# Optimization experiments

Hardware: AMD Instinct MI355X
Metric: run time of the kernel (lower is better)

The kernel has to match this reference:

```python
import jax, jax.numpy as jnp
import numpy as np

B, S, H, D_MODEL, D_HEAD = 2, 2048, 12, 768, 64
INIT_RANGE = 0.02
IGNORE = -100000.0


def setup_inputs() -> dict:
    key = jax.random.key(0)
    ks = jax.random.split(key, 11)
    return {
        "normalized_resid_pre_q": jax.random.normal(ks[0], (B, S, H, D_MODEL), jnp.float32),
        "normalized_resid_pre_k": jax.random.normal(ks[1], (B, S, H, D_MODEL), jnp.float32),
        "normalized_resid_pre_v": jax.random.normal(ks[2], (B, S, H, D_MODEL), jnp.float32),
        "W_Q": jax.random.normal(ks[3], (H, D_MODEL, D_HEAD), jnp.float32) * INIT_RANGE,
        "b_Q": jnp.zeros((H, D_HEAD), jnp.float32),
        "W_K": jax.random.normal(ks[4], (H, D_MODEL, D_HEAD), jnp.float32) * INIT_RANGE,
        "b_K": jnp.zeros((H, D_HEAD), jnp.float32),
        "W_V": jax.random.normal(ks[5], (H, D_MODEL, D_HEAD), jnp.float32) * INIT_RANGE,
        "b_V": jnp.zeros((H, D_HEAD), jnp.float32),
        "W_O": jax.random.normal(ks[6], (H, D_HEAD, D_MODEL), jnp.float32) * INIT_RANGE,
        "b_O": jnp.zeros((D_MODEL,), jnp.float32),
    }


def reference(normalized_resid_pre_q, normalized_resid_pre_k, normalized_resid_pre_v,
              W_Q, b_Q, W_K, b_K, W_V, b_V, W_O, b_O):
    n_heads = W_Q.shape[0]
    d_head = W_Q.shape[-1]
    # per-head projections: input already carries a head axis
    q = jnp.einsum("bqhm,hmd->bqhd", normalized_resid_pre_q, W_Q) + b_Q
    k = jnp.einsum("bkhm,hmd->bkhd", normalized_resid_pre_k, W_K) + b_K
    v = jnp.einsum("bkhm,hmd->bkhd", normalized_resid_pre_v, W_V) + b_V
    scores = jnp.einsum("bqhd,bkhd->bhqk", q, k) / jnp.sqrt(jnp.float32(d_head))
    S_q, S_k = scores.shape[-2], scores.shape[-1]
    causal = jnp.triu(jnp.ones((S_q, S_k), bool), k=1)
    scores = jnp.where(causal, jnp.float32(IGNORE), scores)
    pattern = jax.nn.softmax(scores, axis=-1)
    z = jnp.einsum("bhqk,bkhd->bqhd", pattern, v)
    # output keeps the per-head axis; bias split evenly across heads
    attn_out = jnp.einsum("bqhd,hdm->bqhm", z, W_O) + b_O / n_heads
    return attn_out
```

## Files before the change

kernel.cpp:

```cpp
#include <hip/hip_runtime.h>
#include <stdint.h>

#define H 12
#define S 2048
#define BATCH 2
#define DM 768
#define DH 64

typedef __attribute__((ext_vector_type(4))) float f32x4;
typedef __attribute__((ext_vector_type(4))) short s16x4;
typedef __attribute__((ext_vector_type(8))) short s16x8;

static __device__ __forceinline__ short f2bf(float f) {
  uint32_t u = __builtin_bit_cast(uint32_t, f);
  uint32_t r = (u + 0x7FFFu + ((u >> 16) & 1u)) >> 16;
  return (short)r;
}

static __device__ __forceinline__ f32x4 zero4() {
  f32x4 v; v[0] = 0.f; v[1] = 0.f; v[2] = 0.f; v[3] = 0.f; return v;
}

#define GLD_LDS16(g, l)                                                              \
  __builtin_amdgcn_global_load_lds((__attribute__((address_space(1))) const void*)(g), \
                                   (__attribute__((address_space(3))) void*)(l), 16, 0, 0)

__global__ __launch_bounds__(256) void k_prep(const float* __restrict__ wq,
                                              const float* __restrict__ wk,
                                              const float* __restrict__ wv,
                                              const float* __restrict__ wo,
                                              short* __restrict__ wt,
                                              short* __restrict__ wot) {
  int tid = blockIdx.x * 256 + threadIdx.x;
  int nthr = gridDim.x * 256;
  const int NQKV = 3 * H * DM * DH;
  for (int i = tid; i < NQKV; i += nthr) {
    int n = i & 63;
    int k = (i >> 6) % DM;
    int rest = (i >> 6) / DM;
    int h = rest % H;
    int t = rest / H;
    const float* src = (t == 0 ? wq : t == 1 ? wk : wv);
    float v = src[((size_t)h * DM + k) * DH + n];
    wt[(((size_t)t * H + h) * DH + n) * DM + k] = f2bf(v);
  }
  const int NO = H * DH * DM;
  for (int i = tid; i < NO; i += nthr) {
    int m = i % DM;
    int d = (i / DM) % DH;
    int h = i / (DM * DH);
    wot[((size_t)h * DM + m) * DH + d] = f2bf(wo[((size_t)h * DH + d) * DM + m]);
  }
}

__global__ __launch_bounds__(256) void k_proj(
    const float* __restrict__ xq, const float* __restrict__ xk, const float* __restrict__ xv,
    const float* __restrict__ bq, const float* __restrict__ bk, const float* __restrict__ bv,
    const short* __restrict__ wt,
    short* __restrict__ q_ws, short* __restrict__ k_ws, short* __restrict__ vt_ws) {
  const int t = blockIdx.z;
  const int h = blockIdx.y;
  const int b = blockIdx.x >> 5;
  const int q0 = (blockIdx.x & 31) * 64;

  const float* x = (t == 0 ? xq : t == 1 ? xk : xv);
  const float* xbase = x + ((size_t)(b * S + q0) * H + h) * DM;
  const short* wbase = wt + ((size_t)t * H + h) * (size_t)DH * DM;

  __shared__ short A_sm[64 * 72];
  __shared__ short W_sm[64 * 64];

  const int tid = threadIdx.x;
  const int w = tid >> 6;
  const int l = tid & 63;
  const int g = l >> 4;
  const int m16 = l & 15;
  const int swz_src = ((l & 7) ^ (l >> 3)) * 8;

  f32x4 acc[4];
  for (int nt = 0; nt < 4; ++nt) acc[nt] = zero4();

  for (int kc = 0; kc < 12; ++kc) {
    if (kc) __syncthreads();
    for (int i = 0; i < 2; ++i) {
      int ch = w * 2 + i;
      int n = ch * 8 + (l >> 3);
      GLD_LDS16(wbase + (size_t)n * DM + kc * 64 + swz_src, (char*)W_sm + ch * 1024);
    }
    for (int p = 0; p < 4; ++p) {
      int q = p * 16 + (tid >> 4);
      int k0 = 4 * (tid & 15);
      f32x4 v = *(const f32x4*)(xbase + (size_t)q * (H * DM) + kc * 64 + k0);
      s16x4 o;
      o.x = f2bf(v[0]); o.y = f2bf(v[1]); o.z = f2bf(v[2]); o.w = f2bf(v[3]);
      *(s16x4*)(&A_sm[q * 72 + k0]) = o;
    }
    __syncthreads();
    for (int c = 0; c < 2; ++c) {
      int krow = 8 * g + 32 * c;
      s16x8 a = *(const s16x8*)(&A_sm[(16 * w + m16) * 72 + krow]);
      for (int nt = 0; nt < 4; ++nt) {
        int n = m16 + 16 * nt;
        int byte = (n * 128 + krow * 2) ^ ((n & 7) << 4);
        s16x8 bfr = *(const s16x8*)((const char*)W_sm + byte);
        acc[nt] = __builtin_amdgcn_mfma_f32_16x16x32_bf16(a, bfr, acc[nt], 0, 0, 0);
      }
    }
  }

  const float* bias = (t == 0 ? bq : t == 1 ? bk : bv) + h * DH;
  if (t < 2) {
    short* dst = (t == 0 ? q_ws : k_ws) + (size_t)(b * H + h) * S * DH;
    for (int nt = 0; nt < 4; ++nt) {
      int n = 16 * nt + m16;
      float bb = bias[n];
      for (int r = 0; r < 4; ++r) {
        int q = q0 + 16 * w + 4 * g + r;
        dst[(size_t)q * DH + n] = f2bf(acc[nt][r] + bb);
      }
    }
  } else {
    short* dst = vt_ws + (size_t)(b * H + h) * DH * S;
    for (int nt = 0; nt < 4; ++nt) {
      int n = 16 * nt + m16;
      float bb = bias[n];
      for (int r = 0; r < 4; ++r) {
        int q = q0 + 16 * w + 4 * g + r;
        dst[(size_t)n * S + q] = f2bf(acc[nt][r] + bb);
      }
    }
  }
}

__global__ __launch_bounds__(256) void k_attn(const short* __restrict__ q_ws,
                                              const short* __restrict__ k_ws,
                                              const short* __restrict__ vt_ws,
                                              short* __restrict__ z_ws) {
  const int b = blockIdx.z;
  const int h = blockIdx.y;
  const int q0 = blockIdx.x * 64;

  const size_t sl = (size_t)(b * H + h) * S * DH;
  const short* qs = q_ws + sl;
  const short* ks = k_ws + sl;
  const short* vs = vt_ws + sl;
  short* zs = z_ws + sl;

  __shared__ short K_sm[64 * 64];
  __shared__ short V_sm[64 * 64];
  __shared__ short P_sm[4][16 * 72];

  const int tid = threadIdx.x;
  const int w = tid >> 6;
  const int l = tid & 63;
  const int g = l >> 4;
  const int m16 = l & 15;
  const int swz_src = ((l & 7) ^ (l >> 3)) * 8;

  s16x8 qf[2];
  {
    int q = q0 + 16 * w + m16;
    qf[0] = *(const s16x8*)(qs + (size_t)q * DH + 8 * g);
    qf[1] = *(const s16x8*)(qs + (size_t)q * DH + 8 * g + 32);
  }

  f32x4 o_acc[4];
  float m_run[4], l_run[4], alpha[4];
  for (int nt = 0; nt < 4; ++nt) o_acc[nt] = zero4();
  for (int r = 0; r < 4; ++r) { m_run[r] = -3.0e38f; l_run[r] = 0.f; }

  const int ktiles = (q0 >> 6) + 1;
  for (int kt = 0; kt < ktiles; ++kt) {
    const int kv0 = kt * 64;
    if (kt) __syncthreads();
    for (int i = 0; i < 2; ++i) {
      int ch = w * 2 + i;
      int row = ch * 8 + (l >> 3);
      GLD_LDS16(ks + (size_t)(kv0 + row) * DH + swz_src, (char*)K_sm + ch * 1024);
      GLD_LDS16(vs + (size_t)row * S + kv0 + swz_src, (char*)V_sm + ch * 1024);
    }
    __syncthreads();

    f32x4 sacc[4];
    for (int nt = 0; nt < 4; ++nt) sacc[nt] = zero4();
    for (int c = 0; c < 2; ++c) {
      int kr2 = (8 * g + 32 * c) * 2;
      for (int nt = 0; nt < 4; ++nt) {
        int row = m16 + 16 * nt;
        s16x8 kf = *(const s16x8*)((const char*)K_sm + ((row * 128 + kr2) ^ ((row & 7) << 4)));
        sacc[nt] = __builtin_amdgcn_mfma_f32_16x16x32_bf16(qf[c], kf, sacc[nt], 0, 0, 0);
      }
    }
    float sv[4][4];
    for (int nt = 0; nt < 4; ++nt) {
      int kv = kv0 + 16 * nt + m16;
      for (int r = 0; r < 4; ++r) {
        int q = q0 + 16 * w + 4 * g + r;
        float s = sacc[nt][r] * 0.125f;
        sv[nt][r] = (kv > q) ? -1.0e30f : s;
      }
    }
    for (int r = 0; r < 4; ++r) {
      float tm = fmaxf(fmaxf(sv[0][r], sv[1][r]), fmaxf(sv[2][r], sv[3][r]));
      tm = fmaxf(tm, __shfl_xor(tm, 1));
      tm = fmaxf(tm, __shfl_xor(tm, 2));
      tm = fmaxf(tm, __shfl_xor(tm, 4));
      tm = fmaxf(tm, __shfl_xor(tm, 8));
      float mn = fmaxf(m_run[r], tm);
      alpha[r] = __expf(m_run[r] - mn);
      m_run[r] = mn;
      float rs = 0.f;
      for (int nt = 0; nt < 4; ++nt) {
        float p = __expf(sv[nt][r] - mn);
        sv[nt][r] = p;
        rs += p;
      }
      rs += __shfl_xor(rs, 1);
      rs += __shfl_xor(rs, 2);
      rs += __shfl_xor(rs, 4);
      rs += __shfl_xor(rs, 8);
      l_run[r] = l_run[r] * alpha[r] + rs;
    }
    for (int nt = 0; nt < 4; ++nt)
      for (int r = 0; r < 4; ++r)
        P_sm[w][(4 * g + r) * 72 + 16 * nt + m16] = f2bf(sv[nt][r]);
    for (int nt = 0; nt < 4; ++nt)
      for (int r = 0; r < 4; ++r) o_acc[nt][r] *= alpha[r];
    for (int c = 0; c < 2; ++c) {
      s16x8 pf = *(const s16x8*)(&P_sm[w][m16 * 72 + 8 * g + 32 * c]);
      int kv2 = (8 * g + 32 * c) * 2;
      for (int nt = 0; nt < 4; ++nt) {
        int d = m16 + 16 * nt;
        s16x8 vf = *(const s16x8*)((const char*)V_sm + ((d * 128 + kv2) ^ ((d & 7) << 4)));
        o_acc[nt] = __builtin_amdgcn_mfma_f32_16x16x32_bf16(pf, vf, o_acc[nt], 0, 0, 0);
      }
    }
  }
  for (int nt = 0; nt < 4; ++nt) {
    int d = 16 * nt + m16;
    for (int r = 0; r < 4; ++r) {
      int q = q0 + 16 * w + 4 * g + r;
      zs[(size_t)q * DH + d] = f2bf(o_acc[nt][r] / l_run[r]);
    }
  }
}

__global__ __launch_bounds__(256) void k_oproj(const short* __restrict__ z_ws,
                                               const short* __restrict__ wot,
                                               const float* __restrict__ bo,
                                               float* __restrict__ out) {
  const int b = blockIdx.z;
  const int h = blockIdx.y;
  const int q0 = blockIdx.x * 64;

  const short* zs = z_ws + (size_t)(b * H + h) * S * DH;
  const short* wos = wot + (size_t)h * DM * DH;

  __shared__ short Z_sm[64 * 64];
  __shared__ short W_sm[128 * 64];

  const int tid = threadIdx.x;
  const int w = tid >> 6;
  const int l = tid & 63;
  const int g = l >> 4;
  const int m16 = l & 15;
  const int swz_src = ((l & 7) ^ (l >> 3)) * 8;

  for (int i = 0; i < 2; ++i) {
    int ch = w * 2 + i;
    int row = ch * 8 + (l >> 3);
    GLD_LDS16(zs + (size_t)(q0 + row) * DH + swz_src, (char*)Z_sm + ch * 1024);
  }
  __syncthreads();
  s16x8 af[2];
  for (int c = 0; c < 2; ++c) {
    int row = 16 * w + m16;
    int kr2 = (8 * g + 32 * c) * 2;
    af[c] = *(const s16x8*)((const char*)Z_sm + ((row * 128 + kr2) ^ ((row & 7) << 4)));
  }

  for (int nc = 0; nc < 6; ++nc) {
    const int n0 = nc * 128;
    __syncthreads();
    for (int i = 0; i < 4; ++i) {
      int ch = w * 4 + i;
      int row = ch * 8 + (l >> 3);
      GLD_LDS16(wos + (size_t)(n0 + row) * DH + swz_src, (char*)W_sm + ch * 1024);
    }
    __syncthreads();
    f32x4 acc[8];
    for (int nt = 0; nt < 8; ++nt) acc[nt] = zero4();
    for (int c = 0; c < 2; ++c) {
      int kr2 = (8 * g + 32 * c) * 2;
      for (int nt = 0; nt < 8; ++nt) {
        int row = m16 + 16 * nt;
        s16x8 bf = *(const s16x8*)((const char*)W_sm + ((row * 128 + kr2) ^ ((row & 7) << 4)));
        acc[nt] = __builtin_amdgcn_mfma_f32_16x16x32_bf16(af[c], bf, acc[nt], 0, 0, 0);
      }
    }
    for (int nt = 0; nt < 8; ++nt) {
      int m = n0 + 16 * nt + m16;
      float bias = bo[m] * (1.0f / 12.0f);
      for (int r = 0; r < 4; ++r) {
        int q = q0 + 16 * w + 4 * g + r;
        out[((size_t)(b * S + q) * H + h) * DM + m] = acc[nt][r] + bias;
      }
    }
  }
}

extern "C" void kernel_launch(void* const* d_in, const int* in_sizes, int n_in,
                              void* d_out, int out_size, void* d_ws, size_t ws_size,
                              hipStream_t stream) {
  const float* xq = (const float*)d_in[0];
  const float* xk = (const float*)d_in[1];
  const float* xv = (const float*)d_in[2];
  const float* wq = (const float*)d_in[3];
  const float* bq = (const float*)d_in[4];
  const float* wk = (const float*)d_in[5];
  const float* bk = (const float*)d_in[6];
  const float* wv = (const float*)d_in[7];
  const float* bv = (const float*)d_in[8];
  const float* wo = (const float*)d_in[9];
  const float* bo = (const float*)d_in[10];
  float* out = (float*)d_out;

  short* wt = (short*)d_ws;
  short* wot = wt + (size_t)3 * H * DH * DM;
  short* q_ws = wot + (size_t)H * DM * DH;
  short* k_ws = q_ws + (size_t)BATCH * H * S * DH;
  short* vt_ws = k_ws + (size_t)BATCH * H * S * DH;
  short* z_ws = vt_ws + (size_t)BATCH * H * S * DH;

  k_prep<<<dim3(1024), dim3(256), 0, stream>>>(wq, wk, wv, wo, wt, wot);
  k_proj<<<dim3(64, H, 3), dim3(256), 0, stream>>>(xq, xk, xv, bq, bk, bv, wt, q_ws, k_ws, vt_ws);
  k_attn<<<dim3(32, H, BATCH), dim3(256), 0, stream>>>(q_ws, k_ws, vt_ws, z_ws);
  k_oproj<<<dim3(32, H, BATCH), dim3(256), 0, stream>>>(z_ws, wot, bo, out);
}
```

Measured before the change: 265.6 us.

## Double-buffer LDS tiles, load projection inputs straight to registers, swizzle blocks across XCDs

Result: slower. 277.0 us (+4.3%).

```diff
diff --git a/kernel.cpp b/kernel.cpp
--- a/kernel.cpp
+++ b/kernel.cpp
@@ -1,4 +1,5 @@
 #include <hip/hip_runtime.h>
+#include <hip/hip_bf16.h>
 #include <stdint.h>
 
 #define H 12
@@ -17,13 +18,27 @@
   return (short)r;
 }
 
+static __device__ __forceinline__ s16x8 cvt8(f32x4 a, f32x4 b) {
+  s16x8 r;
+  r[0] = f2bf(a[0]); r[1] = f2bf(a[1]); r[2] = f2bf(a[2]); r[3] = f2bf(a[3]);
+  r[4] = f2bf(b[0]); r[5] = f2bf(b[1]); r[6] = f2bf(b[2]); r[7] = f2bf(b[3]);
+  return r;
+}
+
 static __device__ __forceinline__ f32x4 zero4() {
   f32x4 v; v[0] = 0.f; v[1] = 0.f; v[2] = 0.f; v[3] = 0.f; return v;
+}
+
+static __device__ __forceinline__ int xcd_swz(int lin, int n) {
+  int q = n >> 3;
+  return (lin & 7) * q + (lin >> 3);
 }
 
 #define GLD_LDS16(g, l)                                                              \
   __builtin_amdgcn_global_load_lds((__attribute__((address_space(1))) const void*)(g), \
                                    (__attribute__((address_space(3))) void*)(l), 16, 0, 0)
+
+#define VM_BARRIER() do { asm volatile("s_waitcnt vmcnt(0)" ::: "memory"); __syncthreads(); } while (0)
 
 __global__ __launch_bounds__(256) void k_prep(const float* __restrict__ wq,
                                               const float* __restrict__ wk,
@@ -58,17 +73,18 @@
     const float* __restrict__ bq, const float* __restrict__ bk, const float* __restrict__ bv,
     const short* __restrict__ wt,
     short* __restrict__ q_ws, short* __restrict__ k_ws, short* __restrict__ vt_ws) {
-  const int t = blockIdx.z;
-  const int h = blockIdx.y;
-  const int b = blockIdx.x >> 5;
-  const int q0 = (blockIdx.x & 31) * 64;
+  int lin = blockIdx.x + 64 * (blockIdx.y + 12 * blockIdx.z);
+  lin = xcd_swz(lin, 64 * 12 * 3);
+  const int t = lin / (64 * 12);
+  const int h = (lin >> 6) % 12;
+  const int b = (lin & 63) >> 5;
+  const int q0 = (lin & 31) * 64;
 
   const float* x = (t == 0 ? xq : t == 1 ? xk : xv);
   const float* xbase = x + ((size_t)(b * S + q0) * H + h) * DM;
   const short* wbase = wt + ((size_t)t * H + h) * (size_t)DH * DM;
 
-  __shared__ short A_sm[64 * 72];
-  __shared__ short W_sm[64 * 64];
+  __shared__ short W_sm[2][64 * 64];
 
   const int tid = threadIdx.x;
   const int w = tid >> 6;
@@ -77,43 +93,74 @@
   const int m16 = l & 15;
   const int swz_src = ((l & 7) ^ (l >> 3)) * 8;
 
+  const float* xrow = xbase + (size_t)(16 * w + m16) * (H * DM) + 8 * g;
+
   f32x4 acc[4];
+#pragma unroll
   for (int nt = 0; nt < 4; ++nt) acc[nt] = zero4();
 
-  for (int kc = 0; kc < 12; ++kc) {
-    if (kc) __syncthreads();
-    for (int i = 0; i < 2; ++i) {
-      int ch = w * 2 + i;
-      int n = ch * 8 + (l >> 3);
-      GLD_LDS16(wbase + (size_t)n * DM + kc * 64 + swz_src, (char*)W_sm + ch * 1024);
-    }
-    for (int p = 0; p < 4; ++p) {
-      int q = p * 16 + (tid >> 4);
-      int k0 = 4 * (tid & 15);
-      f32x4 v = *(const f32x4*)(xbase + (size_t)q * (H * DM) + kc * 64 + k0);
-      s16x4 o;
-      o.x = f2bf(v[0]); o.y = f2bf(v[1]); o.z = f2bf(v[2]); o.w = f2bf(v[3]);
-      *(s16x4*)(&A_sm[q * 72 + k0]) = o;
-    }
-    __syncthreads();
-    for (int c = 0; c < 2; ++c) {
-      int krow = 8 * g + 32 * c;
-      s16x8 a = *(const s16x8*)(&A_sm[(16 * w + m16) * 72 + krow]);
-      for (int nt = 0; nt < 4; ++nt) {
-        int n = m16 + 16 * nt;
-        int byte = (n * 128 + krow * 2) ^ ((n & 7) << 4);
-        s16x8 bfr = *(const s16x8*)((const char*)W_sm + byte);
-        acc[nt] = __builtin_amdgcn_mfma_f32_16x16x32_bf16(a, bfr, acc[nt], 0, 0, 0);
-      }
-    }
+#define PROJ_STAGE_W(sel, kc)                                                        \
+  do {                                                                               \
+    _Pragma("unroll") for (int i = 0; i < 2; ++i) {                                  \
+      int ch = w * 2 + i;                                                            \
+      int n = ch * 8 + (l >> 3);                                                     \
+      GLD_LDS16(wbase + (size_t)n * DM + (kc) * 64 + swz_src,                        \
+                (char*)W_sm + (sel) * 8192 + ch * 1024);                             \
+    }                                                                                \
+  } while (0)
+
+#define PROJ_LOAD_A(d0, d1, d2, d3, kc)                                              \
+  do {                                                                               \
+    const float* rp = xrow + (kc) * 64;                                              \
+    d0 = *(const f32x4*)(rp);                                                        \
+    d1 = *(const f32x4*)(rp + 4);                                                    \
+    d2 = *(const f32x4*)(rp + 32);                                                   \
+    d3 = *(const f32x4*)(rp + 36);                                                   \
+  } while (0)
+
+#define PROJ_COMPUTE(sel, A0, A1, A2, A3)                                            \
+  do {                                                                               \
+    s16x8 afr0 = cvt8(A0, A1);                                                       \
+    s16x8 afr1 = cvt8(A2, A3);                                                       \
+    _Pragma("unroll") for (int c = 0; c < 2; ++c) {                                  \
+      int krow = 8 * g + 32 * c;                                                     \
+      _Pragma("unroll") for (int nt = 0; nt < 4; ++nt) {                             \
+        int n = m16 + 16 * nt;                                                       \
+        int byte = (sel) * 8192 + ((n * 128 + krow * 2) ^ ((n & 7) << 4));           \
+        s16x8 bfr = *(const s16x8*)((const char*)W_sm + byte);                       \
+        acc[nt] = __builtin_amdgcn_mfma_f32_16x16x32_bf16(c ? afr1 : afr0, bfr,      \
+                                                          acc[nt], 0, 0, 0);         \
+      }                                                                              \
+    }                                                                                \
+  } while (0)
+
+  f32x4 xa0, xa1, xa2, xa3, xb0, xb1, xb2, xb3;
+  PROJ_STAGE_W(0, 0);
+  PROJ_LOAD_A(xa0, xa1, xa2, xa3, 0);
+  VM_BARRIER();
+  for (int kc = 0; kc < 12; kc += 2) {
+    if (kc + 1 < 12) {
+      PROJ_STAGE_W(1, kc + 1);
+      PROJ_LOAD_A(xb0, xb1, xb2, xb3, kc + 1);
+    }
+    PROJ_COMPUTE(0, xa0, xa1, xa2, xa3);
+    VM_BARRIER();
+    if (kc + 2 < 12) {
+      PROJ_STAGE_W(0, kc + 2);
+      PROJ_LOAD_A(xa0, xa1, xa2, xa3, kc + 2);
+    }
+    PROJ_COMPUTE(1, xb0, xb1, xb2, xb3);
+    VM_BARRIER();
   }
 
   const float* bias = (t == 0 ? bq : t == 1 ? bk : bv) + h * DH;
   if (t < 2) {
     short* dst = (t == 0 ? q_ws : k_ws) + (size_t)(b * H + h) * S * DH;
+#pragma unroll
     for (int nt = 0; nt < 4; ++nt) {
       int n = 16 * nt + m16;
       float bb = bias[n];
+#pragma unroll
       for (int r = 0; r < 4; ++r) {
         int q = q0 + 16 * w + 4 * g + r;
         dst[(size_t)q * DH + n] = f2bf(acc[nt][r] + bb);
@@ -121,9 +168,11 @@
     }
   } else {
     short* dst = vt_ws + (size_t)(b * H + h) * DH * S;
+#pragma unroll
     for (int nt = 0; nt < 4; ++nt) {
       int n = 16 * nt + m16;
       float bb = bias[n];
+#pragma unroll
       for (int r = 0; r < 4; ++r) {
         int q = q0 + 16 * w + 4 * g + r;
         dst[(size_t)n * S + q] = f2bf(acc[nt][r] + bb);
@@ -136,9 +185,11 @@
                                               const short* __restrict__ k_ws,
                                               const short* __restrict__ vt_ws,
                                               short* __restrict__ z_ws) {
-  const int b = blockIdx.z;
-  const int h = blockIdx.y;
-  const int q0 = blockIdx.x * 64;
+  int lin = blockIdx.x + 32 * (blockIdx.y + 12 * blockIdx.z);
+  lin = xcd_swz(lin, 32 * 12 * 2);
+  const int q0 = (lin & 31) * 64;
+  const int h = (lin >> 5) % 12;
+  const int b = lin / (32 * 12);
 
   const size_t sl = (size_t)(b * H + h) * S * DH;
   const short* qs = q_ws + sl;
@@ -146,8 +197,8 @@
   const short* vs = vt_ws + sl;
   short* zs = z_ws + sl;
 
-  __shared__ short K_sm[64 * 64];
-  __shared__ short V_sm[64 * 64];
+  __shared__ short K_sm[2][64 * 64];
+  __shared__ short V_sm[2][64 * 64];
   __shared__ short P_sm[4][16 * 72];
 
   const int tid = threadIdx.x;
@@ -157,6 +208,18 @@
   const int m16 = l & 15;
   const int swz_src = ((l & 7) ^ (l >> 3)) * 8;
 
+#define ATTN_STAGE(sel, kv0)                                                         \
+  do {                                                                               \
+    _Pragma("unroll") for (int i = 0; i < 2; ++i) {                                  \
+      int ch = w * 2 + i;                                                            \
+      int row = ch * 8 + (l >> 3);                                                   \
+      GLD_LDS16(ks + (size_t)((kv0) + row) * DH + swz_src,                           \
+                (char*)K_sm + (sel) * 8192 + ch * 1024);                             \
+      GLD_LDS16(vs + (size_t)row * S + (kv0) + swz_src,                              \
+                (char*)V_sm + (sel) * 8192 + ch * 1024);                             \
+    }                                                                                \
+  } while (0)
+
   s16x8 qf[2];
   {
     int q = q0 + 16 * w + m16;
@@ -166,40 +229,45 @@
 
   f32x4 o_acc[4];
   float m_run[4], l_run[4], alpha[4];
+#pragma unroll
   for (int nt = 0; nt < 4; ++nt) o_acc[nt] = zero4();
+#pragma unroll
   for (int r = 0; r < 4; ++r) { m_run[r] = -3.0e38f; l_run[r] = 0.f; }
 
   const int ktiles = (q0 >> 6) + 1;
+  ATTN_STAGE(0, 0);
+  VM_BARRIER();
   for (int kt = 0; kt < ktiles; ++kt) {
     const int kv0 = kt * 64;
-    if (kt) __syncthreads();
-    for (int i = 0; i < 2; ++i) {
-      int ch = w * 2 + i;
-      int row = ch * 8 + (l >> 3);
-      GLD_LDS16(ks + (size_t)(kv0 + row) * DH + swz_src, (char*)K_sm + ch * 1024);
-      GLD_LDS16(vs + (size_t)row * S + kv0 + swz_src, (char*)V_sm + ch * 1024);
-    }
-    __syncthreads();
+    const int cur = kt & 1;
+    if (kt + 1 < ktiles) ATTN_STAGE(cur ^ 1, kv0 + 64);
 
     f32x4 sacc[4];
+#pragma unroll
     for (int nt = 0; nt < 4; ++nt) sacc[nt] = zero4();
+#pragma unroll
     for (int c = 0; c < 2; ++c) {
       int kr2 = (8 * g + 32 * c) * 2;
+#pragma unroll
       for (int nt = 0; nt < 4; ++nt) {
         int row = m16 + 16 * nt;
-        s16x8 kf = *(const s16x8*)((const char*)K_sm + ((row * 128 + kr2) ^ ((row & 7) << 4)));
+        s16x8 kf = *(const s16x8*)((const char*)K_sm + cur * 8192 +
+                                   ((row * 128 + kr2) ^ ((row & 7) << 4)));
         sacc[nt] = __builtin_amdgcn_mfma_f32_16x16x32_bf16(qf[c], kf, sacc[nt], 0, 0, 0);
       }
     }
     float sv[4][4];
+#pragma unroll
     for (int nt = 0; nt < 4; ++nt) {
       int kv = kv0 + 16 * nt + m16;
+#pragma unroll
       for (int r = 0; r < 4; ++r) {
         int q = q0 + 16 * w + 4 * g + r;
         float s = sacc[nt][r] * 0.125f;
         sv[nt][r] = (kv > q) ? -1.0e30f : s;
       }
     }
+#pragma unroll
     for (int r = 0; r < 4; ++r) {
       float tm = fmaxf(fmaxf(sv[0][r], sv[1][r]), fmaxf(sv[2][r], sv[3][r]));
       tm = fmaxf(tm, __shfl_xor(tm, 1));
@@ -210,6 +278,7 @@
       alpha[r] = __expf(m_run[r] - mn);
       m_run[r] = mn;
       float rs = 0.f;
+#pragma unroll
       for (int nt = 0; nt < 4; ++nt) {
         float p = __expf(sv[nt][r] - mn);
         sv[nt][r] = p;
@@ -221,23 +290,33 @@
       rs += __shfl_xor(rs, 8);
       l_run[r] = l_run[r] * alpha[r] + rs;
     }
+#pragma unroll
     for (int nt = 0; nt < 4; ++nt)
+#pragma unroll
       for (int r = 0; r < 4; ++r)
         P_sm[w][(4 * g + r) * 72 + 16 * nt + m16] = f2bf(sv[nt][r]);
+#pragma unroll
     for (int nt = 0; nt < 4; ++nt)
+#pragma unroll
       for (int r = 0; r < 4; ++r) o_acc[nt][r] *= alpha[r];
+#pragma unroll
     for (int c = 0; c < 2; ++c) {
       s16x8 pf = *(const s16x8*)(&P_sm[w][m16 * 72 + 8 * g + 32 * c]);
       int kv2 = (8 * g + 32 * c) * 2;
+#pragma unroll
       for (int nt = 0; nt < 4; ++nt) {
         int d = m16 + 16 * nt;
-        s16x8 vf = *(const s16x8*)((const char*)V_sm + ((d * 128 + kv2) ^ ((d & 7) << 4)));
+        s16x8 vf = *(const s16x8*)((const char*)V_sm + cur * 8192 +
+                                   ((d * 128 + kv2) ^ ((d & 7) << 4)));
         o_acc[nt] = __builtin_amdgcn_mfma_f32_16x16x32_bf16(pf, vf, o_acc[nt], 0, 0, 0);
       }
     }
-  }
+    VM_BARRIER();
+  }
+#pragma unroll
   for (int nt = 0; nt < 4; ++nt) {
     int d = 16 * nt + m16;
+#pragma unroll
     for (int r = 0; r < 4; ++r) {
       int q = q0 + 16 * w + 4 * g + r;
       zs[(size_t)q * DH + d] = f2bf(o_acc[nt][r] / l_run[r]);
@@ -249,15 +328,17 @@
                                                const short* __restrict__ wot,
                                                const float* __restrict__ bo,
                                                float* __restrict__ out) {
-  const int b = blockIdx.z;
-  const int h = blockIdx.y;
-  const int q0 = blockIdx.x * 64;
+  int lin = blockIdx.x + 32 * (blockIdx.y + 12 * blockIdx.z);
+  lin = xcd_swz(lin, 32 * 12 * 2);
+  const int q0 = (lin & 31) * 64;
+  const int h = (lin >> 5) % 12;
+  const int b = lin / (32 * 12);
 
   const short* zs = z_ws + (size_t)(b * H + h) * S * DH;
   const short* wos = wot + (size_t)h * DM * DH;
 
   __shared__ short Z_sm[64 * 64];
-  __shared__ short W_sm[128 * 64];
+  __shared__ short W_sm[2][128 * 64];
 
   const int tid = threadIdx.x;
   const int w = tid >> 6;
@@ -266,13 +347,27 @@
   const int m16 = l & 15;
   const int swz_src = ((l & 7) ^ (l >> 3)) * 8;
 
+#define OPROJ_STAGE_W(sel, n0)                                                       \
+  do {                                                                               \
+    _Pragma("unroll") for (int i = 0; i < 4; ++i) {                                  \
+      int ch = w * 4 + i;                                                            \
+      int row = ch * 8 + (l >> 3);                                                   \
+      GLD_LDS16(wos + (size_t)((n0) + row) * DH + swz_src,                           \
+                (char*)W_sm + (sel) * 16384 + ch * 1024);                            \
+    }                                                                                \
+  } while (0)
+
+#pragma unroll
   for (int i = 0; i < 2; ++i) {
     int ch = w * 2 + i;
     int row = ch * 8 + (l >> 3);
     GLD_LDS16(zs + (size_t)(q0 + row) * DH + swz_src, (char*)Z_sm + ch * 1024);
   }
-  __syncthreads();
+  OPROJ_STAGE_W(0, 0);
+  VM_BARRIER();
+
   s16x8 af[2];
+#pragma unroll
   for (int c = 0; c < 2; ++c) {
     int row = 16 * w + m16;
     int kr2 = (8 * g + 32 * c) * 2;
@@ -281,31 +376,33 @@
 
   for (int nc = 0; nc < 6; ++nc) {
     const int n0 = nc * 128;
-    __syncthreads();
-    for (int i = 0; i < 4; ++i) {
-      int ch = w * 4 + i;
-      int row = ch * 8 + (l >> 3);
-      GLD_LDS16(wos + (size_t)(n0 + row) * DH + swz_src, (char*)W_sm + ch * 1024);
-    }
-    __syncthreads();
+    const int cur = nc & 1;
+    if (nc + 1 < 6) OPROJ_STAGE_W(cur ^ 1, n0 + 128);
     f32x4 acc[8];
+#pragma unroll
     for (int nt = 0; nt < 8; ++nt) acc[nt] = zero4();
+#pragma unroll
     for (int c = 0; c < 2; ++c) {
       int kr2 = (8 * g + 32 * c) * 2;
+#pragma unroll
       for (int nt = 0; nt < 8; ++nt) {
         int row = m16 + 16 * nt;
-        s16x8 bf = *(const s16x8*)((const char*)W_sm + ((row * 128 + kr2) ^ ((row & 7) << 4)));
+        s16x8 bf = *(const s16x8*)((const char*)W_sm + cur * 16384 +
+                                   ((row * 128 + kr2) ^ ((row & 7) << 4)));
         acc[nt] = __builtin_amdgcn_mfma_f32_16x16x32_bf16(af[c], bf, acc[nt], 0, 0, 0);
       }
     }
+#pragma unroll
     for (int nt = 0; nt < 8; ++nt) {
       int m = n0 + 16 * nt + m16;
       float bias = bo[m] * (1.0f / 12.0f);
+#pragma unroll
       for (int r = 0; r < 4; ++r) {
         int q = q0 + 16 * w + 4 * g + r;
         out[((size_t)(b * S + q) * H + h) * DM + m] = acc[nt][r] + bias;
       }
     }
+    VM_BARRIER();
   }
 }
 
```
